# Kernel optimization log

Hardware: AMD Instinct MI355X
Metric: run time of the kernel (lower is better)

The kernel has to match this reference:

```python
import jax, jax.numpy as jnp
import numpy as np

B = 128        # graphs per batch
N = 512        # nodes per graph (all graphs full-size)
F = 128        # input/hidden feature dim
DEG_AVG = 16   # average degree
E = B * N * DEG_AVG
DEGREES = (3, 3)  # polynomial filter order per conv layer


def setup_inputs() -> dict:
    key = jax.random.key(0)
    ks = jax.random.split(key, 8)
    X = jax.random.normal(ks[0], (B * N, F), dtype=jnp.float32)
    batch = jnp.repeat(jnp.arange(B, dtype=jnp.int32), N)
    # edges constrained within each graph: graph id = e // (N*DEG_AVG)
    gid = jnp.repeat(jnp.arange(B, dtype=jnp.int32), N * DEG_AVG)
    src = jax.random.randint(ks[1], (E,), 0, N, dtype=jnp.int32) + gid * N
    dst = jax.random.randint(ks[2], (E,), 0, N, dtype=jnp.int32) + gid * N
    edge_index = jnp.stack([src, dst], axis=0)
    s = 1.0 / np.sqrt(F)
    W1 = jax.random.normal(ks[3], (F, F), dtype=jnp.float32) * s
    b1 = jnp.zeros((F,), dtype=jnp.float32)
    W2 = jax.random.normal(ks[4], (F, F), dtype=jnp.float32) * s
    b2 = jnp.zeros((F,), dtype=jnp.float32)
    Wr1 = jax.random.normal(ks[5], (F, 64), dtype=jnp.float32) * s
    br1 = jnp.zeros((64,), dtype=jnp.float32)
    Wr2 = jax.random.normal(ks[6], (64, 1), dtype=jnp.float32) * (1.0 / 8.0)
    br2 = jnp.zeros((1,), dtype=jnp.float32)
    return {"X": X, "batch": batch, "edge_index": edge_index,
            "W1": W1, "b1": b1, "W2": W2, "b2": b2,
            "Wr1": Wr1, "br1": br1, "Wr2": Wr2, "br2": br2}


def _build_gso(edge_index):
    # dense per-graph adjacency [B, N, N] (block-diagonal global GSO,
    # represented batched for efficiency)
    g = edge_index[0] // N
    si = edge_index[0] % N
    di = edge_index[1] % N
    A = jnp.zeros((B, N, N), dtype=jnp.float32).at[g, si, di].set(1.0)
    # gso_generator: symmetric degree-normalized adjacency D^-1/2 A D^-1/2
    deg = A.sum(axis=-1)
    dinv = jnp.where(deg > 0, jax.lax.rsqrt(jnp.maximum(deg, 1e-12)), 0.0)
    S = dinv[:, :, None] * A * dinv[:, None, :]
    return S


def _poly_conv(S, x, degree, W, b):
    # sum_{k=0..degree} S^k x, then linear projection
    acc = x
    z = x
    for _ in range(degree):
        z = jnp.einsum('bij,bjf->bif', S, z)
        acc = acc + z
    return jnp.einsum('bnf,fo->bno', acc, W) + b


def reference(X, batch, edge_index, W1, b1, W2, b2, Wr1, br1, Wr2, br2):
    S = _build_gso(edge_index)
    x = X.reshape(B, N, F)  # nodes grouped per graph (batch is sorted)
    x = jax.nn.relu(_poly_conv(S, x, DEGREES[0], W1, b1))
    x = jax.nn.relu(_poly_conv(S, x, DEGREES[1], W2, b2))
    # global mean pool over nodes of each graph
    h = x.mean(axis=1)  # [B, F]
    h = jax.nn.relu(h @ Wr1 + br1)
    out = (h @ Wr2 + br2).squeeze(-1)  # [B]
    return out
```

## Files before the change

kernel.cpp:

```cpp
#include <hip/hip_runtime.h>
#include <hip/hip_bf16.h>

#define NB 128
#define NN 512
#define NF 128
#define BN (NB*NN)
#define NE (BN*16)
#define EPG 8192
#define WPR 16
#define ELLW 64
#define QST 32
#define SST 72
#define WTS 136

typedef short sh8 __attribute__((ext_vector_type(8)));
typedef float f32x4 __attribute__((ext_vector_type(4)));

static __device__ __forceinline__ unsigned short f2bf(float f) {
    unsigned u = __float_as_uint(f);
    u += 0x7fffu + ((u >> 16) & 1u);
    return (unsigned short)(u >> 16);
}

#define DOT2LO(acc_, pk_, one_) \
    asm("v_dot2_f32_bf16 %0, %1, %2, %0" : "+v"(acc_) : "v"(pk_), "v"(one_))

__global__ __launch_bounds__(256) void scatter_bitmap_kernel(
    const int* __restrict__ src, const int* __restrict__ dst,
    unsigned* __restrict__ bmg)
{
    __shared__ unsigned bm[128 * WPR];
    int b = blockIdx.x;
    int g = b >> 2;
    int qr = b & 3;
    int t = threadIdx.x;

    for (int i = t; i < 128 * WPR; i += 256) bm[i] = 0u;
    __syncthreads();

    const int4* sg4 = (const int4*)(src + (size_t)g * EPG);
    const int4* dg4 = (const int4*)(dst + (size_t)g * EPG);
    int lo = qr << 7;
    for (int i = t; i < EPG / 4; i += 256) {
        int4 s4 = sg4[i];
        int4 d4 = dg4[i];
        int s, d;
        s = s4.x & (NN - 1); d = d4.x & (NN - 1);
        if ((s >> 7) == qr) atomicOr(&bm[(s - lo) * WPR + (d >> 5)], 1u << (d & 31));
        s = s4.y & (NN - 1); d = d4.y & (NN - 1);
        if ((s >> 7) == qr) atomicOr(&bm[(s - lo) * WPR + (d >> 5)], 1u << (d & 31));
        s = s4.z & (NN - 1); d = d4.z & (NN - 1);
        if ((s >> 7) == qr) atomicOr(&bm[(s - lo) * WPR + (d >> 5)], 1u << (d & 31));
        s = s4.w & (NN - 1); d = d4.w & (NN - 1);
        if ((s >> 7) == qr) atomicOr(&bm[(s - lo) * WPR + (d >> 5)], 1u << (d & 31));
    }
    __syncthreads();

    unsigned* outg = bmg + ((size_t)g * NN + (size_t)qr * 128) * WPR;
    #pragma unroll
    for (int i = t; i < 128 * WPR / 4; i += 256)
        *(uint4*)&outg[i * 4] = *(const uint4*)&bm[i * 4];
}

__global__ __launch_bounds__(1024) void rank_ell_kernel(
    const unsigned* __restrict__ bmg,
    unsigned short* __restrict__ ell, int* __restrict__ ocnt,
    float* __restrict__ dinvr, int* __restrict__ perm)
{
    __shared__ unsigned short els[256 * SST];
    __shared__ int qp[NN * 4];
    __shared__ int cs[NN];
    __shared__ int rdeg[NN];
    __shared__ int irank[NN];
    __shared__ int prow[NN];
    __shared__ int prk[NN];
    int b = blockIdx.x;
    int g = b >> 1;
    int h = b & 1;
    int t = threadIdx.x;

    {
        int r = t & 511, hf = t >> 9;
        const unsigned* bgr = bmg + ((size_t)g * NN + r) * WPR + hf * 8;
        uint4 a = *(const uint4*)bgr;
        uint4 c = *(const uint4*)(bgr + 4);
        qp[r * 4 + hf * 2]     = __popc(a.x) + __popc(a.y) + __popc(a.z) + __popc(a.w);
        qp[r * 4 + hf * 2 + 1] = __popc(c.x) + __popc(c.y) + __popc(c.z) + __popc(c.w);
    }
    __syncthreads();
    if (t < NN) {
        int d = qp[t * 4] + qp[t * 4 + 1] + qp[t * 4 + 2] + qp[t * 4 + 3];
        cs[t] = (d > ELLW) ? ELLW : d;
    }
    __syncthreads();

    {
        int r = t & 511, hf = t >> 9;
        int deg_r = cs[r];
        const int4* c4 = (const int4*)cs;
        int ib = hf * 64;
        int pcnt = 0;
        #pragma unroll 8
        for (int ii = 0; ii < 64; ++ii) {
            int4 v = c4[ib + ii];
            int i0 = (ib + ii) * 4;
            pcnt += (v.x < deg_r) || (v.x == deg_r && (i0 + 0) < r);
            pcnt += (v.y < deg_r) || (v.y == deg_r && (i0 + 1) < r);
            pcnt += (v.z < deg_r) || (v.z == deg_r && (i0 + 2) < r);
            pcnt += (v.w < deg_r) || (v.w == deg_r && (i0 + 3) < r);
        }
        if (!hf) prk[r] = pcnt;
        __syncthreads();
        if (hf) {
            int rk = prk[r] + pcnt;
            irank[r] = rk;
            rdeg[rk] = deg_r;
            prow[rk] = r;
            if (h == 0) {
                perm[(size_t)g * NN + rk] = r;
                dinvr[(size_t)g * NN + rk] =
                    (deg_r > 0) ? rsqrtf((float)deg_r) : 0.0f;
            }
        }
    }
    __syncthreads();

    if (h == 0 && t < NN / 8) {
        int m = rdeg[t * 8 + 7];
        ocnt[(size_t)g * (NN / 8) + t] = (m + 3) & ~3;
    }

    {
        int rkl = t >> 2;
        int qw  = t & 3;
        int rk  = h * 256 + rkl;
        int row = prow[rk];
        const unsigned* bq = bmg + ((size_t)g * NN + row) * WPR + qw * 4;
        uint4 bv = *(const uint4*)bq;
        unsigned wbits[4] = {bv.x, bv.y, bv.z, bv.w};
        int c = 0;
        #pragma unroll
        for (int j = 0; j < 3; ++j) c += (j < qw) ? qp[row * 4 + j] : 0;
        unsigned short* er = &els[rkl * SST];
        #pragma unroll
        for (int w = 0; w < 4; ++w) {
            unsigned bits = wbits[w];
            while (bits) {
                int j = __ffs(bits) - 1;
                bits &= bits - 1;
                if (c < ELLW) er[c] = (unsigned short)irank[(qw * 4 + w) * 32 + j];
                ++c;
            }
        }
        if (qw == 3) {
            int cc = (c > ELLW) ? ELLW : c;
            for (int p = cc; p < ELLW; ++p) er[p] = (unsigned short)NN;
        }
    }
    __syncthreads();

    unsigned short* outb = ell + ((size_t)g * NN + (size_t)h * 256) * ELLW;
    for (int idx = t; idx < 256 * 8; idx += 1024) {
        int r2 = idx >> 3, sg2 = idx & 7;
        uint4 v = *(const uint4*)&els[r2 * SST + sg2 * 8];
        *(uint4*)&outb[(size_t)r2 * ELLW + sg2 * 8] = v;
    }
}

__global__ __launch_bounds__(512, 4) void poly_fused_kernel(
    const float* __restrict__ xin,
    unsigned short* __restrict__ accout,
    const unsigned short* __restrict__ ell,
    const int* __restrict__ ocnt,
    const float* __restrict__ dinvr,
    const int* __restrict__ perm,
    int permuteIn)
{
    extern __shared__ float lds[];
    unsigned short* w = (unsigned short*)lds;
    float* dsh = lds + ((NN + 1) * QST * 2) / 4;

    int b = blockIdx.x;
    int g = b & 127;
    int q = b >> 7;
    int t = threadIdx.x;
    int wid = t >> 6;
    int qd  = (t >> 2) & 15;
    int fbq = t & 3;

    unsigned one_lo = 0x00003F80u;
    unsigned one_hi = 0x3F800000u;

    if (t < NN) dsh[t] = dinvr[(size_t)g * NN + t];
    if (t < QST) w[NN * QST + t] = 0;

    int rnk[4];
    #pragma unroll
    for (int x = 0; x < 4; ++x) {
        int wl = (x >= 2) ? (7 - wid) : wid;
        rnk[x] = x * 128 + wl * 16 + qd;
    }

    const int* oc = ocnt + (size_t)g * (NN / 8);
    int co[4];
    #pragma unroll
    for (int x = 0; x < 4; ++x) {
        int ob = (rnk[x] - qd) >> 3;
        co[x] = __builtin_amdgcn_readfirstlane(max(oc[ob], oc[ob + 1]));
    }

    int px[4];
    if (permuteIn) {
        const int* pmg = perm + (size_t)g * NN;
        #pragma unroll
        for (int x = 0; x < 4; ++x) px[x] = pmg[rnk[x]];
    } else {
        #pragma unroll
        for (int x = 0; x < 4; ++x) px[x] = rnk[x];
    }

    const float* xg = xin + (size_t)g * NN * NF + q * 32 + fbq * 8;

    float acc[4][8];
    #pragma unroll
    for (int x = 0; x < 4; ++x) {
        int row = px[x];
        float4 a0 = *(const float4*)&xg[(size_t)row * NF];
        float4 a1 = *(const float4*)&xg[(size_t)row * NF + 4];
        acc[x][0] = a0.x; acc[x][1] = a0.y; acc[x][2] = a0.z; acc[x][3] = a0.w;
        acc[x][4] = a1.x; acc[x][5] = a1.y; acc[x][6] = a1.z; acc[x][7] = a1.w;
    }

    __syncthreads();

    #pragma unroll
    for (int x = 0; x < 4; ++x) {
        float di = dsh[rnk[x]];
        unsigned pk[4];
        #pragma unroll
        for (int k = 0; k < 4; ++k) {
            unsigned lo = (unsigned)f2bf(di * acc[x][2 * k]);
            unsigned hi = (unsigned)f2bf(di * acc[x][2 * k + 1]);
            pk[k] = lo | (hi << 16);
        }
        *(uint4*)&w[rnk[x] * QST + fbq * 8] = make_uint4(pk[0], pk[1], pk[2], pk[3]);
    }
    __syncthreads();

    for (int hop = 0; hop < 3; ++hop) {
        unsigned pst[4][4];
        #pragma unroll
        for (int x = 0; x < 4; ++x) {
            const unsigned short* el =
                ell + ((size_t)g * NN + rnk[x]) * ELLW;
            int cnt = co[x];
            float s[8];
            #pragma unroll
            for (int k = 0; k < 8; ++k) s[k] = 0.0f;

            ushort4 cur = *(const ushort4*)el;
            for (int p = 0; p < cnt; p += 4) {
                ushort4 nxt = cur;
                if (p + 4 < cnt) nxt = *(const ushort4*)(el + p + 4);
                uint4 v0 = *(const uint4*)&w[(int)cur.x * QST + fbq * 8];
                uint4 v1 = *(const uint4*)&w[(int)cur.y * QST + fbq * 8];
                uint4 v2 = *(const uint4*)&w[(int)cur.z * QST + fbq * 8];
                uint4 v3 = *(const uint4*)&w[(int)cur.w * QST + fbq * 8];
                unsigned d[4][4] = {{v0.x, v0.y, v0.z, v0.w},
                                    {v1.x, v1.y, v1.z, v1.w},
                                    {v2.x, v2.y, v2.z, v2.w},
                                    {v3.x, v3.y, v3.z, v3.w}};
                #pragma unroll
                for (int n = 0; n < 4; ++n) {
                    #pragma unroll
                    for (int k = 0; k < 4; ++k) {
                        DOT2LO(s[2 * k],     d[n][k], one_lo);
                        DOT2LO(s[2 * k + 1], d[n][k], one_hi);
                    }
                }
                cur = nxt;
            }

            float di = dsh[rnk[x]];
            #pragma unroll
            for (int k = 0; k < 4; ++k) {
                float zlo = di * s[2 * k];
                float zhi = di * s[2 * k + 1];
                acc[x][2 * k]     += zlo;
                acc[x][2 * k + 1] += zhi;
                unsigned lo = (unsigned)f2bf(di * zlo);
                unsigned hi = (unsigned)f2bf(di * zhi);
                pst[x][k] = lo | (hi << 16);
            }
        }
        __syncthreads();
        #pragma unroll
        for (int x = 0; x < 4; ++x) {
            *(uint4*)&w[rnk[x] * QST + fbq * 8] =
                make_uint4(pst[x][0], pst[x][1], pst[x][2], pst[x][3]);
        }
        __syncthreads();
    }

    unsigned short* og = accout + (size_t)g * NN * NF + q * 32 + fbq * 8;
    #pragma unroll
    for (int x = 0; x < 4; ++x) {
        int rr = rnk[x];
        uint4 pk;
        pk.x = (unsigned)f2bf(acc[x][0]) | ((unsigned)f2bf(acc[x][1]) << 16);
        pk.y = (unsigned)f2bf(acc[x][2]) | ((unsigned)f2bf(acc[x][3]) << 16);
        pk.z = (unsigned)f2bf(acc[x][4]) | ((unsigned)f2bf(acc[x][5]) << 16);
        pk.w = (unsigned)f2bf(acc[x][6]) | ((unsigned)f2bf(acc[x][7]) << 16);
        *(uint4*)&og[(size_t)rr * NF] = pk;
    }
}

__global__ __launch_bounds__(256, 2) void gemm_bias_relu_kernel(
    const unsigned short* __restrict__ X,
    const float* __restrict__ W,
    const float* __restrict__ b, float* __restrict__ Y,
    float* __restrict__ partial, int fuse)
{
    __shared__ __align__(16) unsigned short Wt[NF * WTS];
    __shared__ float part[4 * NF];

    int t = threadIdx.x;

    for (int i = t; i < NF * NF / 4; i += 256) {
        int k = i >> 5;
        int n4 = (i & 31) * 4;
        float4 wv = ((const float4*)W)[i];
        Wt[(n4 + 0) * WTS + k] = f2bf(wv.x);
        Wt[(n4 + 1) * WTS + k] = f2bf(wv.y);
        Wt[(n4 + 2) * WTS + k] = f2bf(wv.z);
        Wt[(n4 + 3) * WTS + k] = f2bf(wv.w);
    }
    __syncthreads();

    int lane = t & 63;
    int wid  = t >> 6;
    int quad = lane >> 4;
    int l16  = lane & 15;
    int rowA0 = blockIdx.x * 128 + wid * 32;

    union { uint4 q; sh8 v; } af[2][4];
    #pragma unroll
    for (int m = 0; m < 2; ++m) {
        int r = rowA0 + m * 16 + l16;
        const unsigned short* xr = X + (size_t)r * NF + quad * 8;
        #pragma unroll
        for (int kk = 0; kk < 4; ++kk)
            af[m][kk].q = *(const uint4*)(xr + kk * 32);
    }

    f32x4 acc[2][8];
    #pragma unroll
    for (int m = 0; m < 2; ++m)
        #pragma unroll
        for (int c = 0; c < 8; ++c) acc[m][c] = (f32x4){0.f, 0.f, 0.f, 0.f};

    #pragma unroll
    for (int c = 0; c < 8; ++c) {
        const unsigned short* wb = &Wt[(c * 16 + l16) * WTS + quad * 8];
        #pragma unroll
        for (int kk = 0; kk < 4; ++kk) {
            union { uint4 q; sh8 v; } bf_;
            bf_.q = *(const uint4*)(wb + kk * 32);
            acc[0][c] = __builtin_amdgcn_mfma_f32_16x16x32_bf16(
                af[0][kk].v, bf_.v, acc[0][c], 0, 0, 0);
            acc[1][c] = __builtin_amdgcn_mfma_f32_16x16x32_bf16(
                af[1][kk].v, bf_.v, acc[1][c], 0, 0, 0);
        }
    }

    float psum[8];
    #pragma unroll
    for (int c = 0; c < 8; ++c) psum[c] = 0.0f;

    #pragma unroll
    for (int c = 0; c < 8; ++c) {
        int col = c * 16 + l16;
        float bias = b[col];
        #pragma unroll
        for (int m = 0; m < 2; ++m) {
            #pragma unroll
            for (int reg = 0; reg < 4; ++reg) {
                int r = rowA0 + m * 16 + quad * 4 + reg;
                float v = fmaxf(acc[m][c][reg] + bias, 0.0f);
                if (!fuse) Y[(size_t)r * NF + col] = v;
                psum[c] += v;
            }
        }
    }

    if (fuse) {
        #pragma unroll
        for (int c = 0; c < 8; ++c) {
            float v = psum[c];
            v += __shfl_xor(v, 16);
            v += __shfl_xor(v, 32);
            if (lane < 16) part[wid * NF + c * 16 + lane] = v;
        }
        __syncthreads();
        if (t < NF) {
            float s = part[t] + part[NF + t] + part[2 * NF + t]
                    + part[3 * NF + t];
            partial[(size_t)blockIdx.x * NF + t] = s;
        }
    }
}

__global__ __launch_bounds__(128) void readout_kernel(
    const float* __restrict__ partial,
    const float* __restrict__ Wr1, const float* __restrict__ br1,
    const float* __restrict__ Wr2, const float* __restrict__ br2,
    float* __restrict__ out)
{
    __shared__ float hsh[NF];
    __shared__ float r1[64];

    int g = blockIdx.x;
    int t = threadIdx.x;

    const float* pg = partial + (size_t)g * 4 * NF;
    float s = 0.0f;
    #pragma unroll
    for (int j = 0; j < 4; ++j) s += pg[j * NF + t];
    hsh[t] = s * (1.0f / (float)NN);
    __syncthreads();

    if (t < 64) {
        float a = br1[t];
        #pragma unroll 8
        for (int k = 0; k < NF; ++k) a += hsh[k] * Wr1[k * 64 + t];
        r1[t] = fmaxf(a, 0.0f);
    }
    __syncthreads();

    if (t < 64) {
        float v = r1[t] * Wr2[t];
        #pragma unroll
        for (int off = 32; off; off >>= 1) v += __shfl_down(v, off);
        if (t == 0) out[g] = v + br2[0];
    }
}

extern "C" void kernel_launch(void* const* d_in, const int* in_sizes, int n_in,
                              void* d_out, int out_size, void* d_ws, size_t ws_size,
                              hipStream_t stream)
{
    const float* X    = (const float*)d_in[0];
    const int*   ei   = (const int*)d_in[2];
    const float* W1   = (const float*)d_in[3];
    const float* b1   = (const float*)d_in[4];
    const float* W2   = (const float*)d_in[5];
    const float* b2   = (const float*)d_in[6];
    const float* Wr1  = (const float*)d_in[7];
    const float* br1  = (const float*)d_in[8];
    const float* Wr2  = (const float*)d_in[9];
    const float* br2  = (const float*)d_in[10];
    float* out = (float*)d_out;

    const int* src = ei;
    const int* dst = ei + NE;

    char* ws = (char*)d_ws;
    float*          dinvr   = (float*)(ws);
    int*            ocnt    = (int*)(ws + (size_t)256 * 1024);
    int*            perm    = (int*)(ws + (size_t)512 * 1024);
    float*          partial = (float*)(ws + (size_t)768 * 1024);
    unsigned short* ell     = (unsigned short*)(ws + (size_t)1024 * 1024);
    unsigned*       bmg     = (unsigned*)(ws + (size_t)9216 * 1024);
    unsigned short* buf0    = (unsigned short*)(ws + (size_t)16384 * 1024);
    float*          buf1    = (float*)(ws + (size_t)49152 * 1024);

    scatter_bitmap_kernel<<<NB * 4, 256, 0, stream>>>(src, dst, bmg);
    rank_ell_kernel<<<NB * 2, 1024, 0, stream>>>(bmg, ell, ocnt, dinvr, perm);

    const size_t LDSSZ = (size_t)(NN + 1) * QST * 2 + NN * 4;

    poly_fused_kernel<<<NB * 4, 512, LDSSZ, stream>>>(X, buf0, ell, ocnt,
                                                      dinvr, perm, 1);
    gemm_bias_relu_kernel<<<BN / 128, 256, 0, stream>>>(buf0, W1, b1, buf1,
                                                        partial, 0);

    poly_fused_kernel<<<NB * 4, 512, LDSSZ, stream>>>(buf1, buf0, ell, ocnt,
                                                      dinvr, perm, 0);
    gemm_bias_relu_kernel<<<BN / 128, 256, 0, stream>>>(buf0, W2, b2, buf1,
                                                        partial, 1);

    readout_kernel<<<NB, 128, 0, stream>>>(partial, Wr1, br1, Wr2, br2, out);
}
```

Measured before the change: 218.2 us.

## Fuse bitmap scatter into rank/ELL kernel using shared-memory adjacency bitmap

```diff
diff --git a/kernel.cpp b/kernel.cpp
--- a/kernel.cpp
+++ b/kernel.cpp
@@ -25,63 +25,47 @@
 #define DOT2LO(acc_, pk_, one_) \
     asm("v_dot2_f32_bf16 %0, %1, %2, %0" : "+v"(acc_) : "v"(pk_), "v"(one_))
 
-__global__ __launch_bounds__(256) void scatter_bitmap_kernel(
+__global__ __launch_bounds__(1024) void build_fused_kernel(
     const int* __restrict__ src, const int* __restrict__ dst,
-    unsigned* __restrict__ bmg)
-{
-    __shared__ unsigned bm[128 * WPR];
-    int b = blockIdx.x;
-    int g = b >> 2;
-    int qr = b & 3;
-    int t = threadIdx.x;
-
-    for (int i = t; i < 128 * WPR; i += 256) bm[i] = 0u;
-    __syncthreads();
-
-    const int4* sg4 = (const int4*)(src + (size_t)g * EPG);
-    const int4* dg4 = (const int4*)(dst + (size_t)g * EPG);
-    int lo = qr << 7;
-    for (int i = t; i < EPG / 4; i += 256) {
-        int4 s4 = sg4[i];
-        int4 d4 = dg4[i];
-        int s, d;
-        s = s4.x & (NN - 1); d = d4.x & (NN - 1);
-        if ((s >> 7) == qr) atomicOr(&bm[(s - lo) * WPR + (d >> 5)], 1u << (d & 31));
-        s = s4.y & (NN - 1); d = d4.y & (NN - 1);
-        if ((s >> 7) == qr) atomicOr(&bm[(s - lo) * WPR + (d >> 5)], 1u << (d & 31));
-        s = s4.z & (NN - 1); d = d4.z & (NN - 1);
-        if ((s >> 7) == qr) atomicOr(&bm[(s - lo) * WPR + (d >> 5)], 1u << (d & 31));
-        s = s4.w & (NN - 1); d = d4.w & (NN - 1);
-        if ((s >> 7) == qr) atomicOr(&bm[(s - lo) * WPR + (d >> 5)], 1u << (d & 31));
-    }
-    __syncthreads();
-
-    unsigned* outg = bmg + ((size_t)g * NN + (size_t)qr * 128) * WPR;
-    #pragma unroll
-    for (int i = t; i < 128 * WPR / 4; i += 256)
-        *(uint4*)&outg[i * 4] = *(const uint4*)&bm[i * 4];
-}
-
-__global__ __launch_bounds__(1024) void rank_ell_kernel(
-    const unsigned* __restrict__ bmg,
     unsigned short* __restrict__ ell, int* __restrict__ ocnt,
     float* __restrict__ dinvr, int* __restrict__ perm)
 {
+    __shared__ unsigned bm[NN * WPR];
     __shared__ unsigned short els[256 * SST];
     __shared__ int qp[NN * 4];
     __shared__ int cs[NN];
     __shared__ int rdeg[NN];
     __shared__ int irank[NN];
     __shared__ int prow[NN];
-    __shared__ int prk[NN];
+    int* prk = (int*)els;
     int b = blockIdx.x;
     int g = b >> 1;
     int h = b & 1;
     int t = threadIdx.x;
 
+    for (int i = t; i < NN * WPR; i += 1024) bm[i] = 0u;
+    __syncthreads();
+
+    const int4* sg4 = (const int4*)(src + (size_t)g * EPG);
+    const int4* dg4 = (const int4*)(dst + (size_t)g * EPG);
+    for (int i = t; i < EPG / 4; i += 1024) {
+        int4 s4 = sg4[i];
+        int4 d4 = dg4[i];
+        int s, d;
+        s = s4.x & (NN - 1); d = d4.x & (NN - 1);
+        atomicOr(&bm[s * WPR + (d >> 5)], 1u << (d & 31));
+        s = s4.y & (NN - 1); d = d4.y & (NN - 1);
+        atomicOr(&bm[s * WPR + (d >> 5)], 1u << (d & 31));
+        s = s4.z & (NN - 1); d = d4.z & (NN - 1);
+        atomicOr(&bm[s * WPR + (d >> 5)], 1u << (d & 31));
+        s = s4.w & (NN - 1); d = d4.w & (NN - 1);
+        atomicOr(&bm[s * WPR + (d >> 5)], 1u << (d & 31));
+    }
+    __syncthreads();
+
     {
         int r = t & 511, hf = t >> 9;
-        const unsigned* bgr = bmg + ((size_t)g * NN + r) * WPR + hf * 8;
+        const unsigned* bgr = &bm[r * WPR + hf * 8];
         uint4 a = *(const uint4*)bgr;
         uint4 c = *(const uint4*)(bgr + 4);
         qp[r * 4 + hf * 2]     = __popc(a.x) + __popc(a.y) + __popc(a.z) + __popc(a.w);
@@ -135,8 +119,7 @@
         int qw  = t & 3;
         int rk  = h * 256 + rkl;
         int row = prow[rk];
-        const unsigned* bq = bmg + ((size_t)g * NN + row) * WPR + qw * 4;
-        uint4 bv = *(const uint4*)bq;
+        uint4 bv = *(const uint4*)&bm[row * WPR + qw * 4];
         unsigned wbits[4] = {bv.x, bv.y, bv.z, bv.w};
         int c = 0;
         #pragma unroll
@@ -470,12 +453,11 @@
     int*            perm    = (int*)(ws + (size_t)512 * 1024);
     float*          partial = (float*)(ws + (size_t)768 * 1024);
     unsigned short* ell     = (unsigned short*)(ws + (size_t)1024 * 1024);
-    unsigned*       bmg     = (unsigned*)(ws + (size_t)9216 * 1024);
     unsigned short* buf0    = (unsigned short*)(ws + (size_t)16384 * 1024);
     float*          buf1    = (float*)(ws + (size_t)49152 * 1024);
 
-    scatter_bitmap_kernel<<<NB * 4, 256, 0, stream>>>(src, dst, bmg);
-    rank_ell_kernel<<<NB * 2, 1024, 0, stream>>>(bmg, ell, ocnt, dinvr, perm);
+    build_fused_kernel<<<NB * 2, 1024, 0, stream>>>(src, dst, ell, ocnt,
+                                                    dinvr, perm);
 
     const size_t LDSSZ = (size_t)(NN + 1) * QST * 2 + NN * 4;
 
```

Result: faster. 212.5 us (-2.6%).
